# Kernel optimization log

Hardware: AMD Instinct MI355X
Metric: run time of the kernel (lower is better)

## Reference

```python
import jax, jax.numpy as jnp
import numpy as np

N, E, F, H, C = 100000, 1600000, 128, 128, 16
NEG_SLOPE = 0.01  # torch F.leaky_relu default


def setup_inputs() -> dict:
    key = jax.random.key(0)
    ks = jax.random.split(key, 32)
    inp = {
        "x": jax.random.normal(ks[0], (N, F), jnp.float32),
        "edge_index": jax.random.randint(ks[1], (2, E), 0, N, jnp.int32),
        "edge_weight": jax.random.uniform(ks[2], (E,), jnp.float32),
    }
    def w(k, fan_in, fan_out):
        s = 1.0 / np.sqrt(fan_in)
        return jax.random.uniform(k, (fan_in, fan_out), jnp.float32, -s, s)
    # cell 0: pre 128->128, arma 128->128, sage 128->128
    inp["pre_w0"] = w(ks[3], F, H); inp["pre_b0"] = jnp.zeros((H,), jnp.float32)
    inp["arma_w0"] = w(ks[4], H, H); inp["arma_v0"] = w(ks[5], H, H); inp["arma_b0"] = jnp.zeros((H,), jnp.float32)
    inp["sage_wl0"] = w(ks[6], H, H); inp["sage_bl0"] = jnp.zeros((H,), jnp.float32); inp["sage_wr0"] = w(ks[7], H, H)
    # cell 1: pre 256->128 (cell0 outputs 2H)
    inp["pre_w1"] = w(ks[8], 2 * H, H); inp["pre_b1"] = jnp.zeros((H,), jnp.float32)
    inp["arma_w1"] = w(ks[9], H, H); inp["arma_v1"] = w(ks[10], H, H); inp["arma_b1"] = jnp.zeros((H,), jnp.float32)
    inp["sage_wl1"] = w(ks[11], H, H); inp["sage_bl1"] = jnp.zeros((H,), jnp.float32); inp["sage_wr1"] = w(ks[12], H, H)
    inp["cls_w"] = w(ks[13], 2 * H, C); inp["cls_b"] = jnp.zeros((C,), jnp.float32)
    return inp


def _cell(h, row, col, norm, ew, cnt, n, arma_w, arma_v, arma_b, sage_wl, sage_bl, sage_wr):
    # ARMAConv (num_stacks=1, num_layers=1): relu(A_hat (h W) + h V + b), A_hat = sym-norm adj (no self loops)
    t = h @ arma_w
    agg = jax.ops.segment_sum(norm[:, None] * t[row], col, num_segments=n)
    h1 = jax.nn.leaky_relu(jax.nn.relu(agg + h @ arma_v + arma_b), NEG_SLOPE)
    # SAGEConv (mean aggr of edge-weighted messages): lin_l(mean_j w_ij h_j) + lin_r(h_i)
    s = jax.ops.segment_sum(ew[:, None] * h[row], col, num_segments=n)
    h2 = jax.nn.leaky_relu((s / cnt[:, None]) @ sage_wl + sage_bl + h @ sage_wr, NEG_SLOPE)
    return jax.nn.elu(jnp.concatenate([h1, h2], axis=1))


def reference(x, edge_index, edge_weight,
              pre_w0, pre_b0, arma_w0, arma_v0, arma_b0, sage_wl0, sage_bl0, sage_wr0,
              pre_w1, pre_b1, arma_w1, arma_v1, arma_b1, sage_wl1, sage_bl1, sage_wr1,
              cls_w, cls_b):
    n = x.shape[0]
    row, col = edge_index[0], edge_index[1]  # messages flow row -> col
    # gcn_norm without self loops (ARMAConv)
    deg = jax.ops.segment_sum(edge_weight, col, num_segments=n)
    dinv = jnp.where(deg > 0, 1.0 / jnp.sqrt(jnp.where(deg > 0, deg, 1.0)), 0.0)
    norm = dinv[row] * edge_weight * dinv[col]
    # scatter_mean denominator (edge counts, clamped to 1)
    cnt = jnp.maximum(jax.ops.segment_sum(jnp.ones_like(edge_weight), col, num_segments=n), 1.0)
    h = x  # eval mode: input dropout is identity
    for p in [(pre_w0, pre_b0, arma_w0, arma_v0, arma_b0, sage_wl0, sage_bl0, sage_wr0),
              (pre_w1, pre_b1, arma_w1, arma_v1, arma_b1, sage_wl1, sage_bl1, sage_wr1)]:
        pw, pb = p[0], p[1]
        h = _cell(h @ pw + pb, row, col, norm, edge_weight, cnt, n, *p[2:])
    logits = h @ cls_w + cls_b
    return jax.nn.log_softmax(logits, axis=-1)
```

## Files before the change

### kernel.cpp

```cpp
#include <hip/hip_runtime.h>
#include <hip/hip_bf16.h>
#include <hip/hip_fp16.h>

typedef __bf16 bf16x8 __attribute__((ext_vector_type(8)));
typedef float f32x4 __attribute__((ext_vector_type(4)));
typedef unsigned short ushort_t;
typedef unsigned int uint_t;

#if defined(__has_builtin)
#if __has_builtin(__builtin_amdgcn_global_load_lds)
#define HAS_GLL 1
#endif
#endif

__device__ inline float blo(uint_t v) { return __uint_as_float(v << 16); }
__device__ inline float bhi(uint_t v) { return __uint_as_float(v & 0xffff0000u); }
__device__ inline ushort_t f2b(float f) {
  uint_t u = __float_as_uint(f);
  uint_t r = (u + 0x7fffu + ((u >> 16) & 1u)) >> 16;
  return (ushort_t)r;
}
__device__ inline uint_t pk2(float a, float b) {
  return (uint_t)f2b(a) | ((uint_t)f2b(b) << 16);
}

__device__ inline int swz(int r, int k) { return (r * 128 + k) ^ ((r & 7) << 3); }
__device__ inline int cswz(int r, int k) { return (r * 256 + k) ^ ((r & 7) << 3); }

__device__ inline bf16x8 ldw(const ushort_t* __restrict__ Wt, int c, int k, int lane) {
  return *(const bf16x8*)&Wt[c * 128 + k * 32 + (lane >> 4) * 8];
}

struct WP { const float* p[12]; };
__global__ void wtp_k(WP wp, ushort_t* __restrict__ wt) {
  int b = blockIdx.x;
  int t = threadIdx.x;
  if (b < 11) {
    const float* W = wp.p[b];
    ushort_t* T = wt + (size_t)b * 128 * 128;
    for (int i = 0; i < 64; ++i) {
      int lin = i * 256 + t;
      int k = lin >> 7, c = lin & 127;
      T[c * 128 + k] = f2b(W[lin]);
    }
  } else {
    const float* W = wp.p[11];
    ushort_t* T = wt + (size_t)11 * 128 * 128;
    for (int i = 0; i < 16; ++i) {
      int lin = i * 256 + t;
      int c = lin >> 8, k = lin & 255;
      T[lin] = f2b(W[k * 16 + c]);
    }
  }
}

__global__ __launch_bounds__(256, 2) void prolog_k(
    const int* __restrict__ col, int* __restrict__ bcnt, int E, int NB, int gE,
    const float* __restrict__ Xf, const ushort_t* __restrict__ Wt0,
    const float* __restrict__ bias0, ushort_t* __restrict__ outp, int nrows) {
  __shared__ ushort_t As[128 * 128];
  int b = blockIdx.x;
  int t = threadIdx.x;
  if (b < gE) {
    int* h = (int*)As;
    h[t] = 0;
    __syncthreads();
    int e0 = b * 8192;
#pragma unroll
    for (int j = 0; j < 32; ++j) {
      int e = e0 + j * 256 + t;
      if (e < E) atomicAdd(&h[col[e] >> 9], 1);
    }
    __syncthreads();
    if (t < NB && h[t] > 0) atomicAdd(&bcnt[t], h[t]);
    return;
  }
  int lane = t & 63, wid = t >> 6;
  int wr = wid >> 1, wc = wid & 1;
  int rowBase = (b - gE) * 128;
#pragma unroll
  for (int i = 0; i < 16; ++i) {
    int f = t + i * 256;
    int r = f >> 5, q = f & 31;
    int gr = rowBase + r;
    float4 v = make_float4(0.f, 0.f, 0.f, 0.f);
    if (gr < nrows) v = *(const float4*)&Xf[(size_t)gr * 128 + q * 4];
    uint2 o;
    o.x = pk2(v.x, v.y);
    o.y = pk2(v.z, v.w);
    *(uint2*)&As[swz(r, q * 4)] = o;
  }
  __syncthreads();
  f32x4 acc[4][4] = {};
#pragma unroll
  for (int k = 0; k < 4; ++k) {
    bf16x8 af[4], wf[4];
#pragma unroll
    for (int m = 0; m < 4; ++m)
      af[m] = *(const bf16x8*)&As[swz(wr * 64 + m * 16 + (lane & 15), k * 32 + (lane >> 4) * 8)];
#pragma unroll
    for (int nn = 0; nn < 4; ++nn) wf[nn] = ldw(Wt0, wc * 64 + nn * 16 + (lane & 15), k, lane);
#pragma unroll
    for (int m = 0; m < 4; ++m)
#pragma unroll
      for (int nn = 0; nn < 4; ++nn)
        acc[m][nn] = __builtin_amdgcn_mfma_f32_16x16x32_bf16(af[m], wf[nn], acc[m][nn], 0, 0, 0);
  }
  __syncthreads();
#pragma unroll
  for (int m = 0; m < 4; ++m) {
    int r0 = wr * 64 + m * 16 + (lane >> 4) * 4;
#pragma unroll
    for (int nn = 0; nn < 4; ++nn) {
      int c = wc * 64 + nn * 16 + (lane & 15);
      float bv = bias0[c];
#pragma unroll
      for (int j = 0; j < 4; ++j) As[(r0 + j) * 128 + c] = f2b(acc[m][nn][j] + bv);
    }
  }
  __syncthreads();
#pragma unroll
  for (int i = 0; i < 8; ++i) {
    int idx = t + i * 256;
    int r = idx >> 4, q = idx & 15;
    int gr = rowBase + r;
    if (gr < nrows) *(uint4*)&outp[(size_t)gr * 128 + q * 8] = *(const uint4*)&As[r * 128 + q * 8];
  }
}


__global__ __launch_bounds__(256) void bscan_k(const int* __restrict__ bcnt,
                                               int* __restrict__ bbase, int* __restrict__ cursor,
                                               int* __restrict__ offs, int NB, int N, int E) {
  __shared__ int sd[256];
  int t = threadIdx.x;
  int v = (t < NB) ? bcnt[t] : 0;
  int acc = v;
  sd[t] = v; __syncthreads();
  for (int off = 1; off < 256; off <<= 1) {
    int x = (t >= off) ? sd[t - off] : 0;
    __syncthreads();
    acc += x; sd[t] = acc;
    __syncthreads();
  }
  if (t < NB) { bbase[t] = acc - v; cursor[t] = acc - v; }
  if (t == 0) { bbase[NB] = E; offs[N] = E; }
}

__global__ __launch_bounds__(512) void bscatter_k(
    const int* __restrict__ row, const int* __restrict__ col, const float* __restrict__ ew,
    int* __restrict__ cursor, uint2* __restrict__ eout, int E, int NB) {
  __shared__ int h[256];
  __shared__ int lofs[256];
  __shared__ int lcur[256];
  __shared__ int gbase[256];
  __shared__ int sc[256];
  __shared__ uint2 stage[8192];
  __shared__ int addr[8192];
  int t = threadIdx.x;
  int e0 = blockIdx.x * 8192;
  int cnt = min(8192, E - e0);
  if (t < 256) h[t] = 0;
  __syncthreads();
#pragma unroll
  for (int j = 0; j < 16; ++j) {
    int e = e0 + j * 512 + t;
    if (e < E) atomicAdd(&h[col[e] >> 9], 1);
  }
  __syncthreads();
  int s = (t < 256) ? h[t] : 0;
  int acc = s;
  if (t < 256) sc[t] = s;
  __syncthreads();
  for (int off = 1; off < 256; off <<= 1) {
    int x = (t < 256 && t >= off) ? sc[t - off] : 0;
    __syncthreads();
    if (t < 256) { acc += x; sc[t] = acc; }
    __syncthreads();
  }
  if (t < NB && s > 0) gbase[t] = atomicAdd(&cursor[t], s);
  if (t < 256) { lofs[t] = acc - s; lcur[t] = acc - s; }
  __syncthreads();
#pragma unroll
  for (int j = 0; j < 16; ++j) {
    int e = e0 + j * 512 + t;
    if (e < E) {
      int c = col[e];
      int bk = c >> 9;
      int p = atomicAdd(&lcur[bk], 1);
      uint2 v;
      v.x = ((uint_t)(c & 511) << 17) | (uint_t)row[e];
      v.y = __float_as_uint(ew[e]);
      stage[p] = v;
      addr[p] = gbase[bk] + (p - lofs[bk]);
    }
  }
  __syncthreads();
  for (int i = t; i < cnt; i += 512) eout[addr[i]] = stage[i];
}

__global__ __launch_bounds__(512) void bsort_k(
    const uint2* __restrict__ ein, const int* __restrict__ bbase,
    int* __restrict__ offs, float* __restrict__ dinv, float* __restrict__ cinv,
    uint2* __restrict__ eout, int N) {
  __shared__ int h[512];
  __shared__ int lcur[512];
  __shared__ float degs[512];
  __shared__ int sd[512];
  int t = threadIdx.x, b = blockIdx.x;
  int base = bbase[b], end = bbase[b + 1];
  int cnt = end - base;
  int node0 = b << 9;
  h[t] = 0;
  degs[t] = 0.f;
  __syncthreads();
  for (int i = t; i < cnt; i += 512) {
    uint2 v = ein[base + i];
    int lc = v.x >> 17;
    atomicAdd(&h[lc], 1);
    atomicAdd(&degs[lc], __uint_as_float(v.y));
  }
  __syncthreads();
  int s = h[t];
  int acc = s;
  sd[t] = s; __syncthreads();
  for (int off = 1; off < 512; off <<= 1) {
    int x = (t >= off) ? sd[t - off] : 0;
    __syncthreads();
    acc += x; sd[t] = acc;
    __syncthreads();
  }
  int excl = acc - s;
  lcur[t] = excl;
  int node = node0 + t;
  if (node < N) {
    offs[node] = base + excl;
    float d = degs[t];
    dinv[node] = d > 0.f ? rsqrtf(d) : 0.f;
    cinv[node] = 1.0f / fmaxf((float)s, 1.f);
  }
  __syncthreads();
  for (int i = t; i < cnt; i += 512) {
    uint2 v = ein[base + i];
    int lc = v.x >> 17;
    int p = atomicAdd(&lcur[lc], 1);
    uint2 o;
    o.x = v.x & 0x1FFFF;
    o.y = v.y;
    eout[base + p] = o;
  }
}

__global__ void edgew_k(uint2* __restrict__ sedge, const float* __restrict__ dinv, int E) {
  int e = blockIdx.x * blockDim.x + threadIdx.x;
  if (e < E) {
    uint2 v = sedge[e];
    float ew = __uint_as_float(v.y);
    float wA = dinv[v.x] * ew;
    uint_t lo = (uint_t)__half_as_ushort(__float2half_rn(wA));
    uint_t hi = (uint_t)__half_as_ushort(__float2half_rn(ew));
    sedge[e].y = lo | (hi << 16);
  }
}

__global__ __launch_bounds__(256) void agg_k(
    const uint_t* __restrict__ hp2, const uint2* __restrict__ sedge,
    const float* __restrict__ dinv, const float* __restrict__ cinv,
    const int* __restrict__ offs,
    uint_t* __restrict__ outA, uint_t* __restrict__ outS, int n) {
  int wid = threadIdx.x >> 6;
  int lane = threadIdx.x & 63;
  int half = lane >> 5, li = lane & 31;
  int node = blockIdx.x * 4 + wid;
  if (node >= n) return;
  int s0 = __builtin_amdgcn_readfirstlane(offs[node]);
  int e0 = __builtin_amdgcn_readfirstlane(offs[node + 1]);
  const char* hpb = (const char*)hp2;
  uint_t libase = (uint_t)(li << 3);
  float a0 = 0.f, a1 = 0.f, a2 = 0.f, a3 = 0.f;
  float m0 = 0.f, m1 = 0.f, m2 = 0.f, m3 = 0.f;
  for (int p = s0; p < e0; p += 8) {
    uint2 ed[4];
#pragma unroll
    for (int j = 0; j < 4; ++j) {
      int k = p + 2 * j + half;
      ed[j] = sedge[k < e0 ? k : s0];
    }
#pragma unroll
    for (int j = 0; j < 4; ++j) {
      int k = p + 2 * j + half;
      bool ok = (k < e0);
      uint_t w = ok ? ed[j].y : 0u;
      uint2 v = *(const uint2*)(hpb + ((ed[j].x << 8) | libase));
      float wA = __half2float(__ushort_as_half((ushort_t)(w & 0xffff)));
      float wS = __half2float(__ushort_as_half((ushort_t)(w >> 16)));
      float f0 = blo(v.x), f1 = bhi(v.x), f2 = blo(v.y), f3 = bhi(v.y);
      a0 += wA * f0; a1 += wA * f1; a2 += wA * f2; a3 += wA * f3;
      m0 += wS * f0; m1 += wS * f1; m2 += wS * f2; m3 += wS * f3;
    }
  }
  a0 += __shfl_xor(a0, 32); a1 += __shfl_xor(a1, 32);
  a2 += __shfl_xor(a2, 32); a3 += __shfl_xor(a3, 32);
  m0 += __shfl_xor(m0, 32); m1 += __shfl_xor(m1, 32);
  m2 += __shfl_xor(m2, 32); m3 += __shfl_xor(m3, 32);
  if (half == 0) {
    float dn = dinv[node];
    uint2 o;
    o.x = pk2(dn * a0, dn * a1);
    o.y = pk2(dn * a2, dn * a3);
    *(uint2*)&outA[(size_t)node * 64 + li * 2] = o;
  } else {
    float cn = cinv[node];
    uint2 o;
    o.x = pk2(cn * m0, cn * m1);
    o.y = pk2(cn * m2, cn * m3);
    *(uint2*)&outS[(size_t)node * 64 + li * 2] = o;
  }
}

__device__ inline void stage_tile64(const ushort_t* __restrict__ A, ushort_t* lds,
                                    int rowBase, int wid, int lane) {
  int lr = lane >> 4, lchunk = lane & 15;
#ifdef HAS_GLL
#pragma unroll
  for (int i = 0; i < 4; ++i) {
    int r = wid * 16 + i * 4 + lr;
    int csrc = (lchunk ^ (r & 7)) << 4;
    const char* g = (const char*)A + (((size_t)(rowBase + r)) << 8) + csrc;
    char* l = (char*)lds + ((wid * 16 + i * 4) << 8);
    __builtin_amdgcn_global_load_lds((const __attribute__((address_space(1))) void*)g,
                                     (__attribute__((address_space(3))) void*)l, 16, 0, 0);
  }
#else
#pragma unroll
  for (int i = 0; i < 4; ++i) {
    int r = wid * 16 + i * 4 + lr;
    uint4 v = *(const uint4*)&A[((size_t)(rowBase + r)) * 128 + lchunk * 8];
    *(uint4*)&lds[swz(r, lchunk * 8)] = v;
  }
#endif
}

__device__ inline void stage_wait() {
#ifdef HAS_GLL
  asm volatile("s_waitcnt vmcnt(0)" ::: "memory");
#endif
}

__device__ inline bf16x8 lda64(const ushort_t* lds, int m, int k, int lane) {
  return *(const bf16x8*)&lds[swz(m * 16 + (lane & 15), k * 32 + (lane >> 4) * 8)];
}

template <int TAIL>
__global__ __launch_bounds__(256, 3) void dualfused_k(
    const ushort_t* __restrict__ X, const ushort_t* __restrict__ Y,
    const ushort_t* __restrict__ H,
    const ushort_t* __restrict__ WX, const ushort_t* __restrict__ WXH,
    const ushort_t* __restrict__ WY, const ushort_t* __restrict__ WYH,
    const float* __restrict__ bX, const float* __restrict__ bY,
    const ushort_t* __restrict__ WZ1, const ushort_t* __restrict__ WZ2,
    const float* __restrict__ bZ,
    ushort_t* __restrict__ outH, float* __restrict__ outL, int nrows) {
  __shared__ ushort_t buf[3 * 64 * 128];
  ushort_t* Xs = buf;
  ushort_t* Ys = buf + 64 * 128;
  ushort_t* Hs = buf + 2 * 64 * 128;
  int t = threadIdx.x, lane = t & 63, wid = t >> 6;
  int rowBase = blockIdx.x * 64;
  int c16 = lane & 15;

  stage_tile64(X, Xs, rowBase, wid, lane);
  stage_tile64(Y, Ys, rowBase, wid, lane);
  stage_tile64(H, Hs, rowBase, wid, lane);
  stage_wait();
  __syncthreads();

  f32x4 acc1[4][2] = {};
  f32x4 acc2[4][2] = {};
#pragma unroll
  for (int k = 0; k < 4; ++k) {
    bf16x8 xf[4], yf[4], hf[4], wx[2], whx[2], wy[2], why[2];
#pragma unroll
    for (int m = 0; m < 4; ++m) {
      xf[m] = lda64(Xs, m, k, lane);
      yf[m] = lda64(Ys, m, k, lane);
      hf[m] = lda64(Hs, m, k, lane);
    }
#pragma unroll
    for (int nn = 0; nn < 2; ++nn) {
      int c = wid * 32 + nn * 16 + c16;
      wx[nn] = ldw(WX, c, k, lane);
      whx[nn] = ldw(WXH, c, k, lane);
      wy[nn] = ldw(WY, c, k, lane);
      why[nn] = ldw(WYH, c, k, lane);
    }
#pragma unroll
    for (int m = 0; m < 4; ++m)
#pragma unroll
      for (int nn = 0; nn < 2; ++nn) {
        acc1[m][nn] = __builtin_amdgcn_mfma_f32_16x16x32_bf16(xf[m], wx[nn], acc1[m][nn], 0, 0, 0);
        acc1[m][nn] = __builtin_amdgcn_mfma_f32_16x16x32_bf16(hf[m], whx[nn], acc1[m][nn], 0, 0, 0);
        acc2[m][nn] = __builtin_amdgcn_mfma_f32_16x16x32_bf16(yf[m], wy[nn], acc2[m][nn], 0, 0, 0);
        acc2[m][nn] = __builtin_amdgcn_mfma_f32_16x16x32_bf16(hf[m], why[nn], acc2[m][nn], 0, 0, 0);
      }
  }

  __syncthreads();

#pragma unroll
  for (int m = 0; m < 4; ++m) {
    int r0 = m * 16 + (lane >> 4) * 4;
#pragma unroll
    for (int nn = 0; nn < 2; ++nn) {
      int c = wid * 32 + nn * 16 + c16;
      float bv1 = bX[c];
      float bv2 = bY[c];
#pragma unroll
      for (int j = 0; j < 4; ++j) {
        int r = r0 + j;
        float v1 = fmaxf(acc1[m][nn][j] + bv1, 0.f);
        buf[cswz(r, c)] = f2b(v1);
        float v2 = acc2[m][nn][j] + bv2;
        v2 = v2 > 0.f ? v2 : (__expf(0.01f * v2) - 1.f);
        buf[cswz(r, 128 + c)] = f2b(v2);
      }
    }
  }
  __syncthreads();

  if (TAIL == 0) {
    f32x4 acc3[4][2] = {};
#pragma unroll
    for (int kk = 0; kk < 8; ++kk) {
      const ushort_t* WZ = (kk < 4) ? WZ1 : WZ2;
      int kl = kk & 3;
      bf16x8 af[4], wf[2];
#pragma unroll
      for (int m = 0; m < 4; ++m)
        af[m] = *(const bf16x8*)&buf[cswz(m * 16 + c16, kk * 32 + (lane >> 4) * 8)];
#pragma unroll
      for (int nn = 0; nn < 2; ++nn) wf[nn] = ldw(WZ, wid * 32 + nn * 16 + c16, kl, lane);
#pragma unroll
      for (int m = 0; m < 4; ++m)
#pragma unroll
        for (int nn = 0; nn < 2; ++nn)
          acc3[m][nn] = __builtin_amdgcn_mfma_f32_16x16x32_bf16(af[m], wf[nn], acc3[m][nn], 0, 0, 0);
    }
    ushort_t* Ob = Hs;
#pragma unroll
    for (int m = 0; m < 4; ++m) {
      int r0 = m * 16 + (lane >> 4) * 4;
#pragma unroll
      for (int nn = 0; nn < 2; ++nn) {
        int c = wid * 32 + nn * 16 + c16;
        float bv = bZ[c];
#pragma unroll
        for (int j = 0; j < 4; ++j) Ob[(r0 + j) * 128 + c] = f2b(acc3[m][nn][j] + bv);
      }
    }
    __syncthreads();
#pragma unroll
    for (int i = 0; i < 4; ++i) {
      int idx = t + i * 256;
      int r = idx >> 4, q = idx & 15;
      int gr = rowBase + r;
      if (gr < nrows) *(uint4*)&outH[(size_t)gr * 128 + q * 8] = *(const uint4*)&Ob[r * 128 + q * 8];
    }
  } else {
    f32x4 accc = {};
#pragma unroll
    for (int kk = 0; kk < 8; ++kk) {
      bf16x8 bfr = *(const bf16x8*)&WZ1[c16 * 256 + kk * 32 + (lane >> 4) * 8];
      bf16x8 af = *(const bf16x8*)&buf[cswz(wid * 16 + c16, kk * 32 + (lane >> 4) * 8)];
      accc = __builtin_amdgcn_mfma_f32_16x16x32_bf16(af, bfr, accc, 0, 0, 0);
    }
    float bc = bZ[c16];
#pragma unroll
    for (int j = 0; j < 4; ++j) {
      float lg = accc[j] + bc;
      float mx = lg;
      for (int d = 1; d < 16; d <<= 1) mx = fmaxf(mx, __shfl_xor(mx, d));
      float ex = __expf(lg - mx);
      float sum = ex;
      for (int d = 1; d < 16; d <<= 1) sum += __shfl_xor(sum, d);
      float r_ = (lg - mx) - logf(sum);
      int grow = rowBase + wid * 16 + (lane >> 4) * 4 + j;
      if (grow < nrows) outL[grow * 16 + c16] = r_;
    }
  }
}


extern "C" void kernel_launch(void* const* d_in, const int* in_sizes, int n_in,
                              void* d_out, int out_size, void* d_ws, size_t ws_size,
                              hipStream_t stream) {
  const float* x        = (const float*)d_in[0];
  const int*   eidx     = (const int*)d_in[1];
  const float* ew       = (const float*)d_in[2];
  const float* pre_w0   = (const float*)d_in[3];
  const float* pre_b0   = (const float*)d_in[4];
  const float* arma_w0  = (const float*)d_in[5];
  const float* arma_v0  = (const float*)d_in[6];
  const float* arma_b0  = (const float*)d_in[7];
  const float* sage_wl0 = (const float*)d_in[8];
  const float* sage_bl0 = (const float*)d_in[9];
  const float* sage_wr0 = (const float*)d_in[10];
  const float* pre_w1   = (const float*)d_in[11];
  const float* pre_b1   = (const float*)d_in[12];
  const float* arma_w1  = (const float*)d_in[13];
  const float* arma_v1  = (const float*)d_in[14];
  const float* arma_b1  = (const float*)d_in[15];
  const float* sage_wl1 = (const float*)d_in[16];
  const float* sage_bl1 = (const float*)d_in[17];
  const float* sage_wr1 = (const float*)d_in[18];
  const float* cls_w    = (const float*)d_in[19];
  const float* cls_b    = (const float*)d_in[20];

  const int N = in_sizes[0] / 128;
  const int E = in_sizes[2];
  const int N_pad = ((N + 127) / 128) * 128;
  const int NB = (N + 511) >> 9;
  const int* row = eidx;
  const int* col = eidx + E;

  char* p = (char*)d_ws;
  auto carve = [&](size_t bytes) { char* q = p; p += (bytes + 255) & ~(size_t)255; return q; };
  ushort_t* hp    = (ushort_t*)carve((size_t)N_pad * 128 * 2);
  ushort_t* bufA  = (ushort_t*)carve((size_t)N_pad * 128 * 2);
  ushort_t* bufS  = (ushort_t*)carve((size_t)N_pad * 128 * 2);
  ushort_t* wt    = (ushort_t*)carve(((size_t)11 * 128 * 128 + 16 * 256) * 2);
  uint2*  sedge  = (uint2*)carve((size_t)E * 8);
  uint2*  sedgeT = (uint2*)carve((size_t)E * 8);
  float*  dinv  = (float*)carve((size_t)N * 4);
  float*  cinv  = (float*)carve((size_t)N * 4);
  int*    offs  = (int*)carve((size_t)(N + 1) * 4);
  int*    bcnt  = (int*)carve((size_t)256 * 4);
  int*    bbase = (int*)carve((size_t)257 * 4);
  int*    cursor= (int*)carve((size_t)256 * 4);

  hipMemsetAsync(bcnt, 0, (size_t)256 * 4, stream);

  const int gE = (E + 8191) / 8192;
  const int gB = (N + 127) / 128;
  const int gB64 = (N + 63) / 64;
  const int gA = (N + 3) / 4;
  auto WT = [&](int i) { return wt + (size_t)i * 128 * 128; };

  WP wp;
  wp.p[0] = pre_w0;  wp.p[1] = arma_w0; wp.p[2] = arma_v0;
  wp.p[3] = sage_wl0; wp.p[4] = sage_wr0;
  wp.p[5] = pre_w1;  wp.p[6] = pre_w1 + 128 * 128;
  wp.p[7] = arma_w1; wp.p[8] = arma_v1;
  wp.p[9] = sage_wl1; wp.p[10] = sage_wr1;
  wp.p[11] = cls_w;

  wtp_k<<<12, 256, 0, stream>>>(wp, wt);
  prolog_k<<<gE + gB, 256, 0, stream>>>(col, bcnt, E, NB, gE, x, WT(0), pre_b0, hp, N);
  bscan_k<<<1, 256, 0, stream>>>(bcnt, bbase, cursor, offs, NB, N, E);
  bscatter_k<<<gE, 512, 0, stream>>>(row, col, ew, cursor, sedgeT, E, NB);
  bsort_k<<<NB, 512, 0, stream>>>(sedgeT, bbase, offs, dinv, cinv, sedge, N);
  edgew_k<<<(E + 255) / 256, 256, 0, stream>>>(sedge, dinv, E);

  agg_k<<<gA, 256, 0, stream>>>((const uint_t*)hp, sedge, dinv, cinv, offs,
                                (uint_t*)bufA, (uint_t*)bufS, N);
  dualfused_k<0><<<gB64, 256, 0, stream>>>(bufA, bufS, hp, WT(1), WT(2), WT(3), WT(4),
                                           arma_b0, sage_bl0, WT(5), WT(6), pre_b1,
                                           hp, nullptr, N);
  agg_k<<<gA, 256, 0, stream>>>((const uint_t*)hp, sedge, dinv, cinv, offs,
                                (uint_t*)bufA, (uint_t*)bufS, N);
  dualfused_k<1><<<gB64, 256, 0, stream>>>(bufA, bufS, hp, WT(7), WT(8), WT(9), WT(10),
                                           arma_b1, sage_bl1, WT(11), nullptr, cls_b,
                                           nullptr, (float*)d_out, N);
}
```

Baseline: 354.2 us.

## Fuse neighbor aggregation into per-cell GEMM kernel writing directly to LDS

```diff
diff --git a/kernel.cpp b/kernel.cpp
--- a/kernel.cpp
+++ b/kernel.cpp
@@ -263,61 +263,6 @@
   }
 }
 
-__global__ __launch_bounds__(256) void agg_k(
-    const uint_t* __restrict__ hp2, const uint2* __restrict__ sedge,
-    const float* __restrict__ dinv, const float* __restrict__ cinv,
-    const int* __restrict__ offs,
-    uint_t* __restrict__ outA, uint_t* __restrict__ outS, int n) {
-  int wid = threadIdx.x >> 6;
-  int lane = threadIdx.x & 63;
-  int half = lane >> 5, li = lane & 31;
-  int node = blockIdx.x * 4 + wid;
-  if (node >= n) return;
-  int s0 = __builtin_amdgcn_readfirstlane(offs[node]);
-  int e0 = __builtin_amdgcn_readfirstlane(offs[node + 1]);
-  const char* hpb = (const char*)hp2;
-  uint_t libase = (uint_t)(li << 3);
-  float a0 = 0.f, a1 = 0.f, a2 = 0.f, a3 = 0.f;
-  float m0 = 0.f, m1 = 0.f, m2 = 0.f, m3 = 0.f;
-  for (int p = s0; p < e0; p += 8) {
-    uint2 ed[4];
-#pragma unroll
-    for (int j = 0; j < 4; ++j) {
-      int k = p + 2 * j + half;
-      ed[j] = sedge[k < e0 ? k : s0];
-    }
-#pragma unroll
-    for (int j = 0; j < 4; ++j) {
-      int k = p + 2 * j + half;
-      bool ok = (k < e0);
-      uint_t w = ok ? ed[j].y : 0u;
-      uint2 v = *(const uint2*)(hpb + ((ed[j].x << 8) | libase));
-      float wA = __half2float(__ushort_as_half((ushort_t)(w & 0xffff)));
-      float wS = __half2float(__ushort_as_half((ushort_t)(w >> 16)));
-      float f0 = blo(v.x), f1 = bhi(v.x), f2 = blo(v.y), f3 = bhi(v.y);
-      a0 += wA * f0; a1 += wA * f1; a2 += wA * f2; a3 += wA * f3;
-      m0 += wS * f0; m1 += wS * f1; m2 += wS * f2; m3 += wS * f3;
-    }
-  }
-  a0 += __shfl_xor(a0, 32); a1 += __shfl_xor(a1, 32);
-  a2 += __shfl_xor(a2, 32); a3 += __shfl_xor(a3, 32);
-  m0 += __shfl_xor(m0, 32); m1 += __shfl_xor(m1, 32);
-  m2 += __shfl_xor(m2, 32); m3 += __shfl_xor(m3, 32);
-  if (half == 0) {
-    float dn = dinv[node];
-    uint2 o;
-    o.x = pk2(dn * a0, dn * a1);
-    o.y = pk2(dn * a2, dn * a3);
-    *(uint2*)&outA[(size_t)node * 64 + li * 2] = o;
-  } else {
-    float cn = cinv[node];
-    uint2 o;
-    o.x = pk2(cn * m0, cn * m1);
-    o.y = pk2(cn * m2, cn * m3);
-    *(uint2*)&outS[(size_t)node * 64 + li * 2] = o;
-  }
-}
-
 __device__ inline void stage_tile64(const ushort_t* __restrict__ A, ushort_t* lds,
                                     int rowBase, int wid, int lane) {
   int lr = lane >> 4, lchunk = lane & 15;
@@ -352,9 +297,10 @@
 }
 
 template <int TAIL>
-__global__ __launch_bounds__(256, 3) void dualfused_k(
-    const ushort_t* __restrict__ X, const ushort_t* __restrict__ Y,
-    const ushort_t* __restrict__ H,
+__global__ __launch_bounds__(256, 3) void cellfused_k(
+    const ushort_t* __restrict__ HP,
+    const uint2* __restrict__ sedge, const float* __restrict__ dinv,
+    const float* __restrict__ cinv, const int* __restrict__ offs,
     const ushort_t* __restrict__ WX, const ushort_t* __restrict__ WXH,
     const ushort_t* __restrict__ WY, const ushort_t* __restrict__ WYH,
     const float* __restrict__ bX, const float* __restrict__ bY,
@@ -368,10 +314,59 @@
   int t = threadIdx.x, lane = t & 63, wid = t >> 6;
   int rowBase = blockIdx.x * 64;
   int c16 = lane & 15;
-
-  stage_tile64(X, Xs, rowBase, wid, lane);
-  stage_tile64(Y, Ys, rowBase, wid, lane);
-  stage_tile64(H, Hs, rowBase, wid, lane);
+  int half = lane >> 5, li = lane & 31;
+
+  stage_tile64(HP, Hs, rowBase, wid, lane);
+
+  const char* hpb = (const char*)HP;
+  uint_t libase = (uint_t)(li << 3);
+#pragma unroll 1
+  for (int i = 0; i < 16; ++i) {
+    int r = wid * 16 + i;
+    int node = rowBase + r;
+    if (node >= nrows) break;
+    int s0 = __builtin_amdgcn_readfirstlane(offs[node]);
+    int e0 = __builtin_amdgcn_readfirstlane(offs[node + 1]);
+    float a0 = 0.f, a1 = 0.f, a2 = 0.f, a3 = 0.f;
+    float m0 = 0.f, m1 = 0.f, m2 = 0.f, m3 = 0.f;
+    for (int p = s0; p < e0; p += 8) {
+      uint2 ed[4];
+#pragma unroll
+      for (int j = 0; j < 4; ++j) {
+        int k = p + 2 * j + half;
+        ed[j] = sedge[k < e0 ? k : s0];
+      }
+#pragma unroll
+      for (int j = 0; j < 4; ++j) {
+        int k = p + 2 * j + half;
+        bool ok = (k < e0);
+        uint_t w = ok ? ed[j].y : 0u;
+        uint2 v = *(const uint2*)(hpb + ((ed[j].x << 8) | libase));
+        float wA = __half2float(__ushort_as_half((ushort_t)(w & 0xffff)));
+        float wS = __half2float(__ushort_as_half((ushort_t)(w >> 16)));
+        float f0 = blo(v.x), f1 = bhi(v.x), f2 = blo(v.y), f3 = bhi(v.y);
+        a0 += wA * f0; a1 += wA * f1; a2 += wA * f2; a3 += wA * f3;
+        m0 += wS * f0; m1 += wS * f1; m2 += wS * f2; m3 += wS * f3;
+      }
+    }
+    a0 += __shfl_xor(a0, 32); a1 += __shfl_xor(a1, 32);
+    a2 += __shfl_xor(a2, 32); a3 += __shfl_xor(a3, 32);
+    m0 += __shfl_xor(m0, 32); m1 += __shfl_xor(m1, 32);
+    m2 += __shfl_xor(m2, 32); m3 += __shfl_xor(m3, 32);
+    if (half == 0) {
+      float dn = dinv[node];
+      uint2 o;
+      o.x = pk2(dn * a0, dn * a1);
+      o.y = pk2(dn * a2, dn * a3);
+      *(uint2*)&Xs[swz(r, li * 4)] = o;
+    } else {
+      float cn = cinv[node];
+      uint2 o;
+      o.x = pk2(cn * m0, cn * m1);
+      o.y = pk2(cn * m2, cn * m3);
+      *(uint2*)&Ys[swz(r, li * 4)] = o;
+    }
+  }
   stage_wait();
   __syncthreads();
 
@@ -526,8 +521,7 @@
   char* p = (char*)d_ws;
   auto carve = [&](size_t bytes) { char* q = p; p += (bytes + 255) & ~(size_t)255; return q; };
   ushort_t* hp    = (ushort_t*)carve((size_t)N_pad * 128 * 2);
-  ushort_t* bufA  = (ushort_t*)carve((size_t)N_pad * 128 * 2);
-  ushort_t* bufS  = (ushort_t*)carve((size_t)N_pad * 128 * 2);
+  ushort_t* hpB   = (ushort_t*)carve((size_t)N_pad * 128 * 2);
   ushort_t* wt    = (ushort_t*)carve(((size_t)11 * 128 * 128 + 16 * 256) * 2);
   uint2*  sedge  = (uint2*)carve((size_t)E * 8);
   uint2*  sedgeT = (uint2*)carve((size_t)E * 8);
@@ -543,7 +537,6 @@
   const int gE = (E + 8191) / 8192;
   const int gB = (N + 127) / 128;
   const int gB64 = (N + 63) / 64;
-  const int gA = (N + 3) / 4;
   auto WT = [&](int i) { return wt + (size_t)i * 128 * 128; };
 
   WP wp;
@@ -561,14 +554,10 @@
   bsort_k<<<NB, 512, 0, stream>>>(sedgeT, bbase, offs, dinv, cinv, sedge, N);
   edgew_k<<<(E + 255) / 256, 256, 0, stream>>>(sedge, dinv, E);
 
-  agg_k<<<gA, 256, 0, stream>>>((const uint_t*)hp, sedge, dinv, cinv, offs,
-                                (uint_t*)bufA, (uint_t*)bufS, N);
-  dualfused_k<0><<<gB64, 256, 0, stream>>>(bufA, bufS, hp, WT(1), WT(2), WT(3), WT(4),
-                                           arma_b0, sage_bl0, WT(5), WT(6), pre_b1,
-                                           hp, nullptr, N);
-  agg_k<<<gA, 256, 0, stream>>>((const uint_t*)hp, sedge, dinv, cinv, offs,
-                                (uint_t*)bufA, (uint_t*)bufS, N);
-  dualfused_k<1><<<gB64, 256, 0, stream>>>(bufA, bufS, hp, WT(7), WT(8), WT(9), WT(10),
-                                           arma_b1, sage_bl1, WT(11), nullptr, cls_b,
-                                           nullptr, (float*)d_out, N);
-}
+  cellfused_k<0><<<gB64, 256, 0, stream>>>(hp, sedge, dinv, cinv, offs,
+                                           WT(1), WT(2), WT(3), WT(4), arma_b0, sage_bl0,
+                                           WT(5), WT(6), pre_b1, hpB, nullptr, N);
+  cellfused_k<1><<<gB64, 256, 0, stream>>>(hpB, sedge, dinv, cinv, offs,
+                                           WT(7), WT(8), WT(9), WT(10), arma_b1, sage_bl1,
+                                           WT(11), nullptr, cls_b, nullptr, (float*)d_out, N);
+}
```

New measurement: 452.7 us. 1.28x slower.
